# Kernel tuning notes

Measured on AMD Instinct MI355X. Metric: run time of the kernel, lower is better.

Reference implementation:

```python
import jax, jax.numpy as jnp
import numpy as np

N_NODES, N_EDGES, N_GRAPHS = 500000, 8000000, 4096
IN_SIZE, HIDDEN, OUT_SIZE = 11, 16, 4
FEAT = IN_SIZE + 7  # 18; also the (buggy) truncated sequence length in the original


def setup_inputs() -> dict:
    key = jax.random.key(0)
    ks = jax.random.split(key, 10)
    x = jax.random.normal(ks[0], (N_NODES, IN_SIZE), dtype=jnp.float32)
    edge_index = jax.random.randint(ks[1], (2, N_EDGES), 0, N_NODES)
    edge_attr = jax.random.randint(ks[2], (N_EDGES,), 0, 7)
    batch = jnp.sort(jax.random.randint(ks[3], (N_EDGES,), 0, N_GRAPHS))
    s = 0.1
    W_ih = jax.random.normal(ks[4], (4 * HIDDEN, FEAT), jnp.float32) * s
    W_hh = jax.random.normal(ks[5], (4 * HIDDEN, HIDDEN), jnp.float32) * s
    b_ih = jax.random.normal(ks[6], (4 * HIDDEN,), jnp.float32) * s
    b_hh = jax.random.normal(ks[7], (4 * HIDDEN,), jnp.float32) * s
    W_fc = jax.random.normal(ks[8], (OUT_SIZE, HIDDEN), jnp.float32) * s
    b_fc = jax.random.normal(ks[9], (OUT_SIZE,), jnp.float32) * s
    return {"x": x, "W_ih": W_ih, "W_hh": W_hh, "b_ih": b_ih, "b_hh": b_hh,
            "W_fc": W_fc, "b_fc": b_fc, "edge_index": edge_index,
            "edge_attr": edge_attr, "batch": batch, "num_graphs": N_GRAPHS}


def _forward(x, W_ih, W_hh, b_ih, b_hh, W_fc, b_fc, edge_index, edge_attr, batch, num_graphs):
    E = edge_index.shape[1]
    # Per-edge gather: node_value = x[n1] + x[n2], concat one-hot edge type (width 7)
    feat = jnp.concatenate(
        [x[edge_index[0]] + x[edge_index[1]],
         jax.nn.one_hot(edge_attr, 7, dtype=x.dtype)], axis=1)  # [E, FEAT]
    # Position of edge j within its graph: j - index of first edge of that graph
    first = jnp.searchsorted(batch, jnp.arange(num_graphs))  # [B]
    pos = jnp.arange(E) - first[batch]                        # [E], >= 0 (batch sorted)
    # Faithful to original bug: sequences truncated to first FEAT (=18) timesteps.
    # Out-of-range positions dropped by scatter mode='drop'.
    seq = jnp.zeros((num_graphs, FEAT, FEAT), x.dtype).at[batch, pos].set(feat, mode='drop')
    # Single-layer LSTM (torch gate order i, f, g, o), batch_first
    bias = b_ih + b_hh

    def step(carry, xt):
        h, c = carry
        gates = xt @ W_ih.T + h @ W_hh.T + bias  # [B, 4H]
        i, f, g, o = jnp.split(gates, 4, axis=-1)
        c = jax.nn.sigmoid(f) * c + jax.nn.sigmoid(i) * jnp.tanh(g)
        h = jax.nn.sigmoid(o) * jnp.tanh(c)
        return (h, c), None

    h0 = jnp.zeros((num_graphs, HIDDEN), x.dtype)
    (h, c), _ = jax.lax.scan(step, (h0, h0), jnp.swapaxes(seq, 0, 1))  # [T,B,F] scan
    # fc applied then last timestep taken -> equals fc(h_last)
    return h @ W_fc.T + b_fc  # [B, OUT_SIZE]


def reference(x, W_ih, W_hh, b_ih, b_hh, W_fc, b_fc, edge_index, edge_attr, batch, num_graphs):
    return _forward(x, W_ih, W_hh, b_ih, b_hh, W_fc, b_fc, edge_index, edge_attr, batch, num_graphs)
```

## Files before the change

### kernel.cpp

```cpp
#include <hip/hip_runtime.h>

#define IN_SIZE 11
#define HID 16
#define FEAT 18
#define TSTEPS 18

__device__ __forceinline__ float fast_rcp(float v) { return __builtin_amdgcn_rcpf(v); }

__device__ __forceinline__ float rl(float v, int lane) {
    return __int_as_float(__builtin_amdgcn_readlane(__float_as_int(v), lane));
}

extern "C" __global__ __launch_bounds__(256, 4)
void tgnn_lstm_fused(const float* __restrict__ x,
                     const float* __restrict__ W_ih,
                     const float* __restrict__ W_hh,
                     const float* __restrict__ b_ih,
                     const float* __restrict__ b_hh,
                     const float* __restrict__ W_fc,
                     const float* __restrict__ b_fc,
                     const int* __restrict__ edge_index,
                     const int* __restrict__ edge_attr,
                     const int* __restrict__ batch,
                     float* __restrict__ out,
                     int E, int B)
{
    const int wl  = threadIdx.x & 63;
    const int g   = (blockIdx.x * blockDim.x + threadIdx.x) >> 6;
    const int u   = wl & 15;
    const int r   = wl >> 4;
    const int row = wl;

    float wih[IN_SIZE], whh[HID];
#pragma unroll
    for (int k = 0; k < IN_SIZE; ++k) wih[k] = W_ih[row * FEAT + k];
#pragma unroll
    for (int v = 0; v < HID; ++v) whh[v] = W_hh[row * HID + v];
    const float bias = b_ih[row] + b_hh[row];
    const float wfc  = W_fc[row];
    const float bfc  = b_fc[r];

    const int vt  = g + (wl >> 5);
    const int l32 = wl & 31;
    int lo = 0, hi = E;
    int n = hi - lo;
    while (n > 32) {
        const int p  = lo + (int)(((unsigned)n * (unsigned)l32) >> 5);
        const int bv = batch[p];
        const unsigned long long bal = __ballot(bv < vt);
        const int myc = (wl < 32) ? __popc((unsigned)bal)
                                  : __popc((unsigned)(bal >> 32));
        const int nlo = myc ? (lo + (int)(((unsigned)n * (unsigned)(myc - 1)) >> 5) + 1) : lo;
        const int nhi = (myc < 32) ? (lo + (int)(((unsigned)n * (unsigned)myc) >> 5)) : hi;
        lo = nlo; hi = nhi; n = hi - lo;
    }
    {
        int p = lo + l32; if (p > E - 1) p = E - 1;
        const bool lt = (l32 < n) && (batch[p] < vt);
        const unsigned long long bal = __ballot(lt);
        const int myc = (wl < 32) ? __popc((unsigned)bal)
                                  : __popc((unsigned)(bal >> 32));
        lo += myc;
    }
    const int f0 = __builtin_amdgcn_readlane(lo, 0);
    const int f1 = __builtin_amdgcn_readlane(lo, 32);
    int cnt = f1 - f0;
    cnt = (cnt < 0) ? 0 : ((cnt > TSTEPS) ? TSTEPS : cnt);

    int n1 = 0, n2 = 0, ea = 0;
    if (wl < TSTEPS) {
        int j = f0 + wl;
        if (j > E - 1) j = E - 1;
        n1 = edge_index[j];
        n2 = edge_index[E + j];
        ea = edge_attr[j];
    }

    float f[IN_SIZE];
    {
        const float* xa = x + (long)n1 * IN_SIZE;
        const float* xb = x + (long)n2 * IN_SIZE;
#pragma unroll
        for (int k = 0; k < IN_SIZE; ++k) f[k] = xa[k] + xb[k];
    }
    if (wl >= cnt) {
#pragma unroll
        for (int k = 0; k < IN_SIZE; ++k) f[k] = 0.0f;
    }

    float ain[TSTEPS];
#pragma unroll
    for (int t = 0; t < TSTEPS; ++t) {
        const int eat = __builtin_amdgcn_readlane(ea, t);
        const float w1 = W_ih[row * FEAT + IN_SIZE + eat];
        float a = bias + ((t < cnt) ? w1 : 0.0f);
#pragma unroll
        for (int k = 0; k < IN_SIZE; ++k)
            a = fmaf(rl(f[k], t), wih[k], a);
        ain[t] = a;
    }

    const float sa = (r == 2) ? -2.0f : -1.0f;
    const float ma = (r == 2) ?  2.0f :  1.0f;
    const float oa = (r == 2) ? -1.0f :  0.0f;

    float h = 0.0f, c = 0.0f;
#pragma unroll
    for (int t = 0; t < TSTEPS; ++t) {
        float a;
        if (t == 0) {
            a = ain[0];
        } else {
            float A0 = ain[t], A1 = 0.0f, A2 = 0.0f, A3 = 0.0f;
#pragma unroll
            for (int v = 0; v < HID; v += 4) {
                A0 = fmaf(rl(h, v + 0), whh[v + 0], A0);
                A1 = fmaf(rl(h, v + 1), whh[v + 1], A1);
                A2 = fmaf(rl(h, v + 2), whh[v + 2], A2);
                A3 = fmaf(rl(h, v + 3), whh[v + 3], A3);
            }
            a = (A0 + A1) + (A2 + A3);
        }
        const float act = fmaf(ma, fast_rcp(1.0f + __expf(sa * a)), oa);
        const float s1 = __shfl_xor(act, 16, 64);
        const float s2 = __shfl_xor(act, 32, 64);
        const float s3 = __shfl_xor(s1, 32, 64);
        c = fmaf(s1, c, act * s2);
        const float th = fmaf(2.0f, fast_rcp(1.0f + __expf(-2.0f * c)), -1.0f);
        h = s3 * th;
    }

    const float hb = __shfl(h, u, 64);
    float p = hb * wfc;
#pragma unroll
    for (int m = 8; m >= 1; m >>= 1) p += __shfl_xor(p, m, 16);
    if (u == 0 && g < B) out[g * 4 + r] = p + bfc;
}

extern "C" void kernel_launch(void* const* d_in, const int* in_sizes, int n_in,
                              void* d_out, int out_size, void* d_ws, size_t ws_size,
                              hipStream_t stream) {
    const float* x     = (const float*)d_in[0];
    const float* W_ih  = (const float*)d_in[1];
    const float* W_hh  = (const float*)d_in[2];
    const float* b_ih  = (const float*)d_in[3];
    const float* b_hh  = (const float*)d_in[4];
    const float* W_fc  = (const float*)d_in[5];
    const float* b_fc  = (const float*)d_in[6];
    const int* edge_index = (const int*)d_in[7];
    const int* edge_attr  = (const int*)d_in[8];
    const int* batch      = (const int*)d_in[9];

    const int E = in_sizes[8];
    const int B = out_size / 4;

    const int grid = (B + 3) / 4;
    tgnn_lstm_fused<<<grid, 256, 0, stream>>>(x, W_ih, W_hh, b_ih, b_hh,
                                              W_fc, b_fc,
                                              edge_index, edge_attr, batch,
                                              (float*)d_out, E, B);
}
```

Baseline: 23.63 us.

## Search a strided sample table of batch before refining within one stripe

A new pre-kernel copies every 128th entry of the sorted batch array into a compact table in workspace. The fused kernel binary-searches that small, cache-friendly table and then resolves the exact graph start with one vectorized int4 load of the 128-entry stripe plus a lane reduction. This replaces several dependent scattered global loads per wave. The cost is an extra kernel launch and a dependency on workspace, and the int4 read near the array end may go out of bounds.

Measured after the change: 27.92 us. 1.18x slower.

```diff
diff --git a/kernel.cpp b/kernel.cpp
--- a/kernel.cpp
+++ b/kernel.cpp
@@ -4,11 +4,20 @@
 #define HID 16
 #define FEAT 18
 #define TSTEPS 18
+#define SSTRIDE 128
 
 __device__ __forceinline__ float fast_rcp(float v) { return __builtin_amdgcn_rcpf(v); }
 
 __device__ __forceinline__ float rl(float v, int lane) {
     return __int_as_float(__builtin_amdgcn_readlane(__float_as_int(v), lane));
+}
+
+__global__ __launch_bounds__(256)
+void sample_batch(const int* __restrict__ batch, int* __restrict__ tbl,
+                  int E, int S)
+{
+    const int i = blockIdx.x * blockDim.x + threadIdx.x;
+    if (i < S) tbl[i] = batch[(long)i * SSTRIDE];
 }
 
 extern "C" __global__ __launch_bounds__(256, 4)
@@ -22,8 +31,9 @@
                      const int* __restrict__ edge_index,
                      const int* __restrict__ edge_attr,
                      const int* __restrict__ batch,
+                     const int* __restrict__ tbl,
                      float* __restrict__ out,
-                     int E, int B)
+                     int E, int B, int S)
 {
     const int wl  = threadIdx.x & 63;
     const int g   = (blockIdx.x * blockDim.x + threadIdx.x) >> 6;
@@ -42,11 +52,11 @@
 
     const int vt  = g + (wl >> 5);
     const int l32 = wl & 31;
-    int lo = 0, hi = E;
+    int lo = 0, hi = S;
     int n = hi - lo;
     while (n > 32) {
-        const int p  = lo + (int)(((unsigned)n * (unsigned)l32) >> 5);
-        const int bv = batch[p];
+        int p = lo + (int)(((unsigned)n * (unsigned)l32) >> 5);
+        const int bv = tbl[p];
         const unsigned long long bal = __ballot(bv < vt);
         const int myc = (wl < 32) ? __popc((unsigned)bal)
                                   : __popc((unsigned)(bal >> 32));
@@ -55,15 +65,27 @@
         lo = nlo; hi = nhi; n = hi - lo;
     }
     {
-        int p = lo + l32; if (p > E - 1) p = E - 1;
-        const bool lt = (l32 < n) && (batch[p] < vt);
+        int p = lo + l32; if (p > S - 1) p = S - 1;
+        const bool lt = (l32 < n) && (tbl[p] < vt);
         const unsigned long long bal = __ballot(lt);
         const int myc = (wl < 32) ? __popc((unsigned)bal)
                                   : __popc((unsigned)(bal >> 32));
         lo += myc;
     }
-    const int f0 = __builtin_amdgcn_readlane(lo, 0);
-    const int f1 = __builtin_amdgcn_readlane(lo, 32);
+    const int istar = lo;
+    const int base  = (istar > 0) ? (istar - 1) * SSTRIDE : 0;
+    int4 q;
+    {
+        const int4* bp = reinterpret_cast<const int4*>(batch + base);
+        q = bp[l32];
+    }
+    int cown = (q.x < vt) + (q.y < vt) + (q.z < vt) + (q.w < vt);
+#pragma unroll
+    for (int m = 16; m >= 1; m >>= 1) cown += __shfl_xor(cown, m, 32);
+    const int lb = (istar == 0) ? 0 : (base + cown);
+
+    const int f0 = __builtin_amdgcn_readlane(lb, 0);
+    const int f1 = __builtin_amdgcn_readlane(lb, 32);
     int cnt = f1 - f0;
     cnt = (cnt < 0) ? 0 : ((cnt > TSTEPS) ? TSTEPS : cnt);
 
@@ -153,10 +175,15 @@
 
     const int E = in_sizes[8];
     const int B = out_size / 4;
+    const int S = (E + SSTRIDE - 1) / SSTRIDE;
+
+    int* tbl = (int*)d_ws;
+
+    sample_batch<<<(S + 255) / 256, 256, 0, stream>>>(batch, tbl, E, S);
 
     const int grid = (B + 3) / 4;
     tgnn_lstm_fused<<<grid, 256, 0, stream>>>(x, W_ih, W_hh, b_ih, b_hh,
                                               W_fc, b_fc,
-                                              edge_index, edge_attr, batch,
-                                              (float*)d_out, E, B);
+                                              edge_index, edge_attr, batch, tbl,
+                                              (float*)d_out, E, B, S);
 }
```

## Precompute graph segment boundaries with a streaming scan kernel instead of per-wave binary search

Applied to the files above, without the earlier changes.

Adds a pre-pass kernel that reads the sorted batch array once with vector loads and writes the first edge index of every graph into workspace. The main LSTM kernel then reads two boundaries per graph instead of running a ballot-based binary search over the batch array. This removes the dependent-load search latency but adds a full pass over the large batch array and an extra kernel launch.

Result: slower. 27.18 us (+15.0%).

```diff
diff --git a/kernel.cpp b/kernel.cpp
--- a/kernel.cpp
+++ b/kernel.cpp
@@ -11,19 +11,62 @@
     return __int_as_float(__builtin_amdgcn_readlane(__float_as_int(v), lane));
 }
 
+__global__ __launch_bounds__(256)
+void scan_bounds(const int* __restrict__ batch, int* __restrict__ first_arr,
+                 int E, int B)
+{
+    const long long t = blockIdx.x * (long long)blockDim.x + threadIdx.x;
+    const long long base = t * 16;
+    if (base >= E) return;
+    const int prev = (base == 0) ? -1 : batch[base - 1];
+
+    if (base + 16 <= E) {
+        const int4* bp = reinterpret_cast<const int4*>(batch + base);
+        const int4 q0 = bp[0], q1 = bp[1], q2 = bp[2], q3 = bp[3];
+        if (q3.w > prev) {
+            int v[17];
+            v[0] = prev;
+            v[1]  = q0.x; v[2]  = q0.y; v[3]  = q0.z; v[4]  = q0.w;
+            v[5]  = q1.x; v[6]  = q1.y; v[7]  = q1.z; v[8]  = q1.w;
+            v[9]  = q2.x; v[10] = q2.y; v[11] = q2.z; v[12] = q2.w;
+            v[13] = q3.x; v[14] = q3.y; v[15] = q3.z; v[16] = q3.w;
+#pragma unroll
+            for (int s = 1; s <= 16; ++s) {
+                if (v[s] > v[s - 1]) {
+                    const int j = (int)base + s - 1;
+                    for (int g2 = v[s - 1] + 1; g2 <= v[s]; ++g2)
+                        first_arr[g2] = j;
+                }
+            }
+        }
+    } else {
+        int pv = prev;
+        for (long long j = base; j < E; ++j) {
+            const int bv = batch[j];
+            if (bv > pv)
+                for (int g2 = pv + 1; g2 <= bv; ++g2) first_arr[g2] = (int)j;
+            pv = bv;
+        }
+    }
+    if (base + 16 >= E) {
+        const int bl = batch[E - 1];
+        for (int g2 = bl + 1; g2 <= B; ++g2) first_arr[g2] = E;
+    }
+}
+
 extern "C" __global__ __launch_bounds__(256, 4)
-void tgnn_lstm_fused(const float* __restrict__ x,
-                     const float* __restrict__ W_ih,
-                     const float* __restrict__ W_hh,
-                     const float* __restrict__ b_ih,
-                     const float* __restrict__ b_hh,
-                     const float* __restrict__ W_fc,
-                     const float* __restrict__ b_fc,
-                     const int* __restrict__ edge_index,
-                     const int* __restrict__ edge_attr,
-                     const int* __restrict__ batch,
-                     float* __restrict__ out,
-                     int E, int B)
+void tgnn_lstm_main(const float* __restrict__ x,
+                    const float* __restrict__ W_ih,
+                    const float* __restrict__ W_hh,
+                    const float* __restrict__ b_ih,
+                    const float* __restrict__ b_hh,
+                    const float* __restrict__ W_fc,
+                    const float* __restrict__ b_fc,
+                    const int* __restrict__ edge_index,
+                    const int* __restrict__ edge_attr,
+                    const int* __restrict__ first_arr,
+                    float* __restrict__ out,
+                    int E, int B)
 {
     const int wl  = threadIdx.x & 63;
     const int g   = (blockIdx.x * blockDim.x + threadIdx.x) >> 6;
@@ -40,30 +83,8 @@
     const float wfc  = W_fc[row];
     const float bfc  = b_fc[r];
 
-    const int vt  = g + (wl >> 5);
-    const int l32 = wl & 31;
-    int lo = 0, hi = E;
-    int n = hi - lo;
-    while (n > 32) {
-        const int p  = lo + (int)(((unsigned)n * (unsigned)l32) >> 5);
-        const int bv = batch[p];
-        const unsigned long long bal = __ballot(bv < vt);
-        const int myc = (wl < 32) ? __popc((unsigned)bal)
-                                  : __popc((unsigned)(bal >> 32));
-        const int nlo = myc ? (lo + (int)(((unsigned)n * (unsigned)(myc - 1)) >> 5) + 1) : lo;
-        const int nhi = (myc < 32) ? (lo + (int)(((unsigned)n * (unsigned)myc) >> 5)) : hi;
-        lo = nlo; hi = nhi; n = hi - lo;
-    }
-    {
-        int p = lo + l32; if (p > E - 1) p = E - 1;
-        const bool lt = (l32 < n) && (batch[p] < vt);
-        const unsigned long long bal = __ballot(lt);
-        const int myc = (wl < 32) ? __popc((unsigned)bal)
-                                  : __popc((unsigned)(bal >> 32));
-        lo += myc;
-    }
-    const int f0 = __builtin_amdgcn_readlane(lo, 0);
-    const int f1 = __builtin_amdgcn_readlane(lo, 32);
+    const int f0 = first_arr[g];
+    const int f1 = first_arr[g + 1];
     int cnt = f1 - f0;
     cnt = (cnt < 0) ? 0 : ((cnt > TSTEPS) ? TSTEPS : cnt);
 
@@ -154,9 +175,15 @@
     const int E = in_sizes[8];
     const int B = out_size / 4;
 
+    int* first_arr = (int*)d_ws;
+
+    const int nthr  = (E + 15) / 16;
+    const int sgrid = (nthr + 255) / 256;
+    scan_bounds<<<sgrid, 256, 0, stream>>>(batch, first_arr, E, B);
+
     const int grid = (B + 3) / 4;
-    tgnn_lstm_fused<<<grid, 256, 0, stream>>>(x, W_ih, W_hh, b_ih, b_hh,
-                                              W_fc, b_fc,
-                                              edge_index, edge_attr, batch,
-                                              (float*)d_out, E, B);
+    tgnn_lstm_main<<<grid, 256, 0, stream>>>(x, W_ih, W_hh, b_ih, b_hh,
+                                             W_fc, b_fc,
+                                             edge_index, edge_attr, first_arr,
+                                             (float*)d_out, E, B);
 }
```
